# Kernel tuning notes

Hardware: AMD Instinct MI355X
Metric: run time of the kernel (lower is better)

The kernel has to match this reference:

```python
import jax, jax.numpy as jnp
import numpy as np

DIM = 192
NUM_HEADS = 6
WS = 8  # window size
N = WS * WS
HEAD_DIM = DIM // NUM_HEADS
SCALE = HEAD_DIM ** -0.5
B_ = 4096  # B * num_windows = 4 * (256/8)^2


def _relative_position_index(ws):
    # Static Swin relative-position index, computed with numpy at trace time.
    coords = np.stack(np.meshgrid(np.arange(ws), np.arange(ws), indexing='ij'))  # (2, ws, ws)
    flat = coords.reshape(2, -1)                       # (2, N)
    rel = flat[:, :, None] - flat[:, None, :]          # (2, N, N)
    rel = rel.transpose(1, 2, 0).astype(np.int64)      # (N, N, 2)
    rel[:, :, 0] += ws - 1
    rel[:, :, 1] += ws - 1
    rel[:, :, 0] *= 2 * ws - 1
    return np.clip(rel.sum(-1), -1000, 1000)           # (N, N)


_REL_IDX = _relative_position_index(WS)


def setup_inputs() -> dict:
    key = jax.random.key(0)
    ks = jax.random.split(key, 6)
    inv = 1.0 / np.sqrt(DIM)
    return {
        'x': jax.random.normal(ks[0], (B_, N, DIM), dtype=jnp.float32),
        'qkv_w': jax.random.normal(ks[1], (3 * DIM, DIM), dtype=jnp.float32) * inv,
        'qkv_b': jax.random.normal(ks[2], (3 * DIM,), dtype=jnp.float32) * 0.02,
        'proj_w': jax.random.normal(ks[3], (DIM, DIM), dtype=jnp.float32) * inv,
        'proj_b': jax.random.normal(ks[4], (DIM,), dtype=jnp.float32) * 0.02,
        'rel_bias_table': jax.random.normal(ks[5], ((2 * WS - 1) ** 2, NUM_HEADS), dtype=jnp.float32) * 0.02,
    }


def reference(x, qkv_w, qkv_b, proj_w, proj_b, rel_bias_table):
    B, n, C = x.shape  # (B_, 64, 192)
    # QKV projection (torch Linear: x @ W^T + b)
    qkv = x @ qkv_w.T + qkv_b                               # (B_, N, 3C)
    qkv = qkv.reshape(B, n, 3, NUM_HEADS, HEAD_DIM)
    qkv = jnp.transpose(qkv, (2, 0, 3, 1, 4))               # (3, B_, h, N, d)
    q, k, v = qkv[0], qkv[1], qkv[2]
    q = q * SCALE
    attn = jnp.einsum('bhnd,bhmd->bhnm', q, k)              # (B_, h, N, N)
    # relative position bias gather: (N*N,) -> (N, N, h) -> (h, N, N)
    bias = rel_bias_table[_REL_IDX.reshape(-1)].reshape(n, n, NUM_HEADS)
    attn = attn + jnp.transpose(bias, (2, 0, 1))[None]
    attn = jax.nn.softmax(attn, axis=-1)
    out = jnp.einsum('bhnm,bhmd->bhnd', attn, v)            # (B_, h, N, d)
    out = jnp.transpose(out, (0, 2, 1, 3)).reshape(B, n, C)
    out = out @ proj_w.T + proj_b
    return out
```

## Files before the change

kernel.cpp:

```cpp
#include <hip/hip_runtime.h>
#include <hip/hip_bf16.h>

#define NWIN 4096
#define NH 6
#define NTOK 64
#define CDIM 192
#define SCALE 0.17677669529663687f
#define LOG2E 1.4426950408889634f

typedef __attribute__((ext_vector_type(8))) short short8;
typedef __attribute__((ext_vector_type(4))) short short4v;
typedef __attribute__((ext_vector_type(4))) float f32x4;

#define MFMA32(A, B, C) __builtin_amdgcn_mfma_f32_16x16x32_bf16(A, B, C, 0, 0, 0)
#define MFMA16(A, B, C) __builtin_amdgcn_mfma_f32_16x16x16bf16_1k(A, B, C, 0, 0, 0)

__device__ __forceinline__ short bf(float x) {
  union { __hip_bfloat16 h; short s; } u;
  u.h = __float2bfloat16(x);
  return u.s;
}

__device__ __forceinline__ short8 cvt8v(f32x4 a, f32x4 b) {
  short8 r;
#pragma unroll
  for (int i = 0; i < 4; ++i) { r[i] = bf(a[i]); r[4 + i] = bf(b[i]); }
  return r;
}

__global__ void prep_weights(const float* __restrict__ qkv_w,
                             const float* __restrict__ proj_w,
                             const float* __restrict__ rel_tbl,
                             const float* __restrict__ qkv_b,
                             short* __restrict__ wbuf,
                             float* __restrict__ biasS,
                             float* __restrict__ qkvb2) {
  const int i = blockIdx.x * 256 + threadIdx.x;
  if (i < 110592) {
    float v = qkv_w[i];
    if (i < 36864) v *= SCALE * LOG2E;
    wbuf[i] = bf(v);
  } else if (i < 147456) {
    wbuf[i] = bf(proj_w[i - 110592]);
  } else if (i < 245760) {
    const int j = i - 147456;
    const int h = j >> 14;
    const int t = j & 16383;
    const int slot = t >> 10;
    const int ln = (t >> 2) & 63;
    const int e = t & 3;
    const int qh = slot >> 3, nl = (slot >> 2) & 1, mt = slot & 3;
    const int n = qh * 32 + nl * 16 + (ln & 15);
    const int m = mt * 16 + (ln >> 4) * 4 + e;
    const int idx = ((n >> 3) - (m >> 3) + 7) * 15 + ((n & 7) - (m & 7) + 7);
    biasS[j] = rel_tbl[idx * NH + h] * LOG2E;
  } else {
    const int j = i - 245760;
    if (j < 576) qkvb2[j] = qkv_b[j] * (j < CDIM ? SCALE * LOG2E : 1.0f);
  }
}

#define LDAF(dst, kc) do {                                              \
  _Pragma("unroll")                                                     \
  for (int mt_ = 0; mt_ < 4; ++mt_) {                                   \
    const int r_ = mt_ * 16 + cc;                                       \
    dst[mt_] = *(const short8*)&lds[r_ * CDIM + ((kc) ^ ((r_ & 7) << 3))]; \
  } } while (0)

__global__ __launch_bounds__(384, 3)
void swin_block_kernel(const float* __restrict__ x,
                       const short* __restrict__ wall,
                       const float* __restrict__ qkvb2,
                       const float* __restrict__ proj_b,
                       const float* __restrict__ biasS,
                       float* __restrict__ out) {
  __shared__ __align__(16) short lds[12288];

  const int b = blockIdx.x;
  const int tid = threadIdx.x;
  const int w = tid >> 6;
  const int lane = tid & 63;
  const int g = lane >> 4;
  const int cc = lane & 15;

  const float* xp = x + (size_t)b * (NTOK * CDIM);

  const int rq0 = (w * 32 + cc) * CDIM;
  const int rq1 = rq0 + 16 * CDIM;
  const short* wk_ = wall + CDIM * CDIM;
  const short* wv_ = wall + 2 * CDIM * CDIM;
  const short* wp_ = wall + 3 * CDIM * CDIM;

#pragma unroll
  for (int it = 0; it < 2; ++it) {
    const int flat = (tid + it * 384) * 16;
    const int r = flat / CDIM;
    const int c = flat % CDIM;
    const int X = (r & 7) << 3;
    f32x4 a0 = *(const f32x4*)(xp + flat);
    f32x4 a1 = *(const f32x4*)(xp + flat + 4);
    f32x4 a2 = *(const f32x4*)(xp + flat + 8);
    f32x4 a3 = *(const f32x4*)(xp + flat + 12);
    *(short8*)&lds[r * CDIM + (c ^ X)] = cvt8v(a0, a1);
    *(short8*)&lds[r * CDIM + ((c + 8) ^ X)] = cvt8v(a2, a3);
  }
  __syncthreads();

  short4v qf[4][2], kf[4][2];
  short4v vf[2][4];

  {
    f32x4 acc[2][4];
#pragma unroll
    for (int ft = 0; ft < 2; ++ft)
#pragma unroll
      for (int mt = 0; mt < 4; ++mt)
        acc[ft][mt] = (f32x4){0.f, 0.f, 0.f, 0.f};
#pragma unroll 1
    for (int ks = 0; ks < 6; ++ks) {
      const int c0 = ks * 32 + g * 8;
      short8 w0 = *(const short8*)&wall[rq0 + c0];
      short8 w1 = *(const short8*)&wall[rq1 + c0];
      short8 afr[4];
      LDAF(afr, c0);
#pragma unroll
      for (int mt = 0; mt < 4; ++mt) {
        acc[0][mt] = MFMA32(w0, afr[mt], acc[0][mt]);
        acc[1][mt] = MFMA32(w1, afr[mt], acc[1][mt]);
      }
    }
#pragma unroll
    for (int ft = 0; ft < 2; ++ft) {
      f32x4 qb = *(const f32x4*)&qkvb2[w * 32 + ft * 16 + g * 4];
#pragma unroll
      for (int nt = 0; nt < 4; ++nt)
#pragma unroll
        for (int j = 0; j < 4; ++j)
          qf[nt][ft][j] = bf(acc[ft][nt][j] + qb[j]);
    }
  }

  {
    f32x4 acc[2][4];
#pragma unroll
    for (int ft = 0; ft < 2; ++ft)
#pragma unroll
      for (int mt = 0; mt < 4; ++mt)
        acc[ft][mt] = (f32x4){0.f, 0.f, 0.f, 0.f};
#pragma unroll 1
    for (int ks = 0; ks < 6; ++ks) {
      const int c0 = ks * 32 + g * 8;
      short8 w0 = *(const short8*)&wk_[rq0 + c0];
      short8 w1 = *(const short8*)&wk_[rq1 + c0];
      short8 afr[4];
      LDAF(afr, c0);
#pragma unroll
      for (int mt = 0; mt < 4; ++mt) {
        acc[0][mt] = MFMA32(w0, afr[mt], acc[0][mt]);
        acc[1][mt] = MFMA32(w1, afr[mt], acc[1][mt]);
      }
    }
#pragma unroll
    for (int ft = 0; ft < 2; ++ft) {
      f32x4 kb = *(const f32x4*)&qkvb2[CDIM + w * 32 + ft * 16 + g * 4];
#pragma unroll
      for (int nt = 0; nt < 4; ++nt)
#pragma unroll
        for (int j = 0; j < 4; ++j)
          kf[nt][ft][j] = bf(acc[ft][nt][j] + kb[j]);
    }
  }

  {
    f32x4 acc[4][2];
#pragma unroll
    for (int mt = 0; mt < 4; ++mt)
#pragma unroll
      for (int dt = 0; dt < 2; ++dt)
        acc[mt][dt] = (f32x4){0.f, 0.f, 0.f, 0.f};
#pragma unroll 1
    for (int ks = 0; ks < 6; ++ks) {
      const int c0 = ks * 32 + g * 8;
      short8 w0 = *(const short8*)&wv_[rq0 + c0];
      short8 w1 = *(const short8*)&wv_[rq1 + c0];
      short8 afr[4];
      LDAF(afr, c0);
#pragma unroll
      for (int mt = 0; mt < 4; ++mt) {
        acc[mt][0] = MFMA32(afr[mt], w0, acc[mt][0]);
        acc[mt][1] = MFMA32(afr[mt], w1, acc[mt][1]);
      }
    }
    float vb0 = qkvb2[2 * CDIM + w * 32 + cc];
    float vb1 = qkvb2[2 * CDIM + w * 32 + 16 + cc];
#pragma unroll
    for (int kt = 0; kt < 4; ++kt)
#pragma unroll
      for (int j = 0; j < 4; ++j) {
        vf[0][kt][j] = bf(acc[kt][0][j] + vb0);
        vf[1][kt][j] = bf(acc[kt][1][j] + vb1);
      }
  }

  __syncthreads();

  const float* bs = biasS + w * 16384;
#pragma unroll
  for (int qh = 0; qh < 2; ++qh) {
    f32x4 sacc[4][2];
#pragma unroll
    for (int mt = 0; mt < 4; ++mt)
#pragma unroll
      for (int nl = 0; nl < 2; ++nl) {
        f32x4 z = *(const f32x4*)&bs[(((qh * 2 + nl) << 2) + mt) * 1024 + lane * 4];
        z = MFMA16(kf[mt][0], qf[qh * 2 + nl][0], z);
        sacc[mt][nl] = MFMA16(kf[mt][1], qf[qh * 2 + nl][1], z);
      }

    short4v pf[2][4];
#pragma unroll
    for (int nl = 0; nl < 2; ++nl) {
      float sum = 0.f;
#pragma unroll
      for (int mt = 0; mt < 4; ++mt)
#pragma unroll
        for (int e = 0; e < 4; ++e) {
          float p = exp2f(sacc[mt][nl][e]);
          sacc[mt][nl][e] = p;
          sum += p;
        }
      sum += __shfl_xor(sum, 16);
      sum += __shfl_xor(sum, 32);
      const float rinv = __builtin_amdgcn_rcpf(sum);
#pragma unroll
      for (int kt = 0; kt < 4; ++kt)
#pragma unroll
        for (int j = 0; j < 4; ++j)
          pf[nl][kt][j] = bf(sacc[kt][nl][j] * rinv);
    }

    f32x4 oacc[2][2];
#pragma unroll
    for (int nl = 0; nl < 2; ++nl)
#pragma unroll
      for (int dt = 0; dt < 2; ++dt) {
        f32x4 z = (f32x4){0.f, 0.f, 0.f, 0.f};
#pragma unroll
        for (int kt = 0; kt < 4; ++kt)
          z = MFMA16(pf[nl][kt], vf[dt][kt], z);
        oacc[nl][dt] = z;
      }

#pragma unroll
    for (int nl = 0; nl < 2; ++nl)
#pragma unroll
      for (int dt = 0; dt < 2; ++dt)
#pragma unroll
        for (int e = 0; e < 4; ++e) {
          const int r = qh * 32 + nl * 16 + g * 4 + e;
          const int c = w * 32 + dt * 16 + cc;
          lds[r * CDIM + (c ^ ((r & 7) << 3))] = bf(oacc[nl][dt][e]);
        }
  }
  __syncthreads();

  f32x4 pacc[4][2];
#pragma unroll
  for (int mt = 0; mt < 4; ++mt)
#pragma unroll
    for (int jt = 0; jt < 2; ++jt)
      pacc[mt][jt] = (f32x4){0.f, 0.f, 0.f, 0.f};

#pragma unroll 1
  for (int ks = 0; ks < 6; ++ks) {
    const int c0 = ks * 32 + g * 8;
    short8 p0 = *(const short8*)&wp_[rq0 + c0];
    short8 p1 = *(const short8*)&wp_[rq1 + c0];
    short8 afr[4];
    LDAF(afr, c0);
#pragma unroll
    for (int mt = 0; mt < 4; ++mt) {
      pacc[mt][0] = MFMA32(p0, afr[mt], pacc[mt][0]);
      pacc[mt][1] = MFMA32(p1, afr[mt], pacc[mt][1]);
    }
  }

  float* op = out + (size_t)b * (NTOK * CDIM);
  f32x4 pbv[2];
  pbv[0] = *(const f32x4*)&proj_b[w * 32 + g * 4];
  pbv[1] = *(const f32x4*)&proj_b[w * 32 + 16 + g * 4];
#pragma unroll
  for (int mt = 0; mt < 4; ++mt)
#pragma unroll
    for (int jt = 0; jt < 2; ++jt) {
      f32x4 v = pacc[mt][jt] + pbv[jt];
      *(f32x4*)&op[(mt * 16 + cc) * CDIM + w * 32 + jt * 16 + g * 4] = v;
    }
}

extern "C" void kernel_launch(void* const* d_in, const int* in_sizes, int n_in,
                              void* d_out, int out_size, void* d_ws, size_t ws_size,
                              hipStream_t stream) {
  const float* x       = (const float*)d_in[0];
  const float* qkv_w   = (const float*)d_in[1];
  const float* qkv_b   = (const float*)d_in[2];
  const float* proj_w  = (const float*)d_in[3];
  const float* proj_b  = (const float*)d_in[4];
  const float* rel_tbl = (const float*)d_in[5];
  float* out = (float*)d_out;

  short* wbuf  = (short*)d_ws;
  float* biasS = (float*)(wbuf + 147456);
  float* qkvb2 = biasS + 98304;

  prep_weights<<<963, 256, 0, stream>>>(qkv_w, proj_w, rel_tbl, qkv_b,
                                        wbuf, biasS, qkvb2);
  swin_block_kernel<<<NWIN, 384, 0, stream>>>(x, wbuf, qkvb2, proj_b, biasS, out);
}
```

Measured before the change: 274.7 us.

## Halve block to three waves, each wave processing two heads with software overlap

The fused Swin window-attention block now uses 192 threads (3 waves) instead of 384, with each wave computing QKV and attention for two heads. The second head's QKV projection is issued before the LDS barrier, so it can overlap with the first head's attention results held in registers. The output projection gives each wave 64 output columns. The aim is to raise blocks per CU and reuse the LDS A-fragments across more MFMAs. The cost is higher register pressure and less parallelism within each block.

```diff
diff --git a/kernel.cpp b/kernel.cpp
--- a/kernel.cpp
+++ b/kernel.cpp
@@ -67,7 +67,176 @@
     dst[mt_] = *(const short8*)&lds[r_ * CDIM + ((kc) ^ ((r_ & 7) << 3))]; \
   } } while (0)
 
-__global__ __launch_bounds__(384, 3)
+__device__ __forceinline__ void stage1_head(
+    const short* lds, const short* wall, const float* qkvb2,
+    int h, int cc, int g,
+    short4v qf[4][2], short4v kf[4][2], short4v vf[2][4]) {
+  const short* wk_ = wall + CDIM * CDIM;
+  const short* wv_ = wall + 2 * CDIM * CDIM;
+  const int r0 = (h * 32 + cc) * CDIM;
+  const int r1 = r0 + 16 * CDIM;
+
+  {
+    f32x4 acc[2][4];
+#pragma unroll
+    for (int ft = 0; ft < 2; ++ft)
+#pragma unroll
+      for (int mt = 0; mt < 4; ++mt)
+        acc[ft][mt] = (f32x4){0.f, 0.f, 0.f, 0.f};
+#pragma unroll 1
+    for (int ks = 0; ks < 6; ++ks) {
+      const int c0 = ks * 32 + g * 8;
+      short8 w0 = *(const short8*)&wall[r0 + c0];
+      short8 w1 = *(const short8*)&wall[r1 + c0];
+      short8 afr[4];
+      LDAF(afr, c0);
+#pragma unroll
+      for (int mt = 0; mt < 4; ++mt) {
+        acc[0][mt] = MFMA32(w0, afr[mt], acc[0][mt]);
+        acc[1][mt] = MFMA32(w1, afr[mt], acc[1][mt]);
+      }
+    }
+#pragma unroll
+    for (int ft = 0; ft < 2; ++ft) {
+      f32x4 qb = *(const f32x4*)&qkvb2[h * 32 + ft * 16 + g * 4];
+#pragma unroll
+      for (int nt = 0; nt < 4; ++nt)
+#pragma unroll
+        for (int j = 0; j < 4; ++j)
+          qf[nt][ft][j] = bf(acc[ft][nt][j] + qb[j]);
+    }
+  }
+  {
+    f32x4 acc[2][4];
+#pragma unroll
+    for (int ft = 0; ft < 2; ++ft)
+#pragma unroll
+      for (int mt = 0; mt < 4; ++mt)
+        acc[ft][mt] = (f32x4){0.f, 0.f, 0.f, 0.f};
+#pragma unroll 1
+    for (int ks = 0; ks < 6; ++ks) {
+      const int c0 = ks * 32 + g * 8;
+      short8 w0 = *(const short8*)&wk_[r0 + c0];
+      short8 w1 = *(const short8*)&wk_[r1 + c0];
+      short8 afr[4];
+      LDAF(afr, c0);
+#pragma unroll
+      for (int mt = 0; mt < 4; ++mt) {
+        acc[0][mt] = MFMA32(w0, afr[mt], acc[0][mt]);
+        acc[1][mt] = MFMA32(w1, afr[mt], acc[1][mt]);
+      }
+    }
+#pragma unroll
+    for (int ft = 0; ft < 2; ++ft) {
+      f32x4 kb = *(const f32x4*)&qkvb2[CDIM + h * 32 + ft * 16 + g * 4];
+#pragma unroll
+      for (int nt = 0; nt < 4; ++nt)
+#pragma unroll
+        for (int j = 0; j < 4; ++j)
+          kf[nt][ft][j] = bf(acc[ft][nt][j] + kb[j]);
+    }
+  }
+  {
+    f32x4 acc[4][2];
+#pragma unroll
+    for (int mt = 0; mt < 4; ++mt)
+#pragma unroll
+      for (int dt = 0; dt < 2; ++dt)
+        acc[mt][dt] = (f32x4){0.f, 0.f, 0.f, 0.f};
+#pragma unroll 1
+    for (int ks = 0; ks < 6; ++ks) {
+      const int c0 = ks * 32 + g * 8;
+      short8 w0 = *(const short8*)&wv_[r0 + c0];
+      short8 w1 = *(const short8*)&wv_[r1 + c0];
+      short8 afr[4];
+      LDAF(afr, c0);
+#pragma unroll
+      for (int mt = 0; mt < 4; ++mt) {
+        acc[mt][0] = MFMA32(afr[mt], w0, acc[mt][0]);
+        acc[mt][1] = MFMA32(afr[mt], w1, acc[mt][1]);
+      }
+    }
+    float vb0 = qkvb2[2 * CDIM + h * 32 + cc];
+    float vb1 = qkvb2[2 * CDIM + h * 32 + 16 + cc];
+#pragma unroll
+    for (int kt = 0; kt < 4; ++kt)
+#pragma unroll
+      for (int j = 0; j < 4; ++j) {
+        vf[0][kt][j] = bf(acc[kt][0][j] + vb0);
+        vf[1][kt][j] = bf(acc[kt][1][j] + vb1);
+      }
+  }
+}
+
+__device__ __forceinline__ void attn_head(
+    const float* biasS, int h, int lane,
+    const short4v qf[4][2], const short4v kf[4][2], const short4v vf[2][4],
+    short4v o[2][2][2]) {
+  const float* bs = biasS + h * 16384;
+#pragma unroll
+  for (int qh = 0; qh < 2; ++qh) {
+    f32x4 sacc[4][2];
+#pragma unroll
+    for (int mt = 0; mt < 4; ++mt)
+#pragma unroll
+      for (int nl = 0; nl < 2; ++nl) {
+        f32x4 z = *(const f32x4*)&bs[(((qh * 2 + nl) << 2) + mt) * 1024 + lane * 4];
+        z = MFMA16(kf[mt][0], qf[qh * 2 + nl][0], z);
+        sacc[mt][nl] = MFMA16(kf[mt][1], qf[qh * 2 + nl][1], z);
+      }
+    short4v pf[2][4];
+#pragma unroll
+    for (int nl = 0; nl < 2; ++nl) {
+      float sum = 0.f;
+#pragma unroll
+      for (int mt = 0; mt < 4; ++mt)
+#pragma unroll
+        for (int e = 0; e < 4; ++e) {
+          float p = exp2f(sacc[mt][nl][e]);
+          sacc[mt][nl][e] = p;
+          sum += p;
+        }
+      sum += __shfl_xor(sum, 16);
+      sum += __shfl_xor(sum, 32);
+      const float rinv = __builtin_amdgcn_rcpf(sum);
+#pragma unroll
+      for (int kt = 0; kt < 4; ++kt)
+#pragma unroll
+        for (int j = 0; j < 4; ++j)
+          pf[nl][kt][j] = bf(sacc[kt][nl][j] * rinv);
+    }
+#pragma unroll
+    for (int nl = 0; nl < 2; ++nl)
+#pragma unroll
+      for (int dt = 0; dt < 2; ++dt) {
+        f32x4 z = (f32x4){0.f, 0.f, 0.f, 0.f};
+#pragma unroll
+        for (int kt = 0; kt < 4; ++kt)
+          z = MFMA16(pf[nl][kt], vf[dt][kt], z);
+#pragma unroll
+        for (int e = 0; e < 4; ++e)
+          o[qh][nl][dt][e] = bf(z[e]);
+      }
+  }
+}
+
+__device__ __forceinline__ void write_ao(short* lds, int h, int g, int cc,
+                                         const short4v o[2][2][2]) {
+#pragma unroll
+  for (int qh = 0; qh < 2; ++qh)
+#pragma unroll
+    for (int nl = 0; nl < 2; ++nl)
+#pragma unroll
+      for (int dt = 0; dt < 2; ++dt)
+#pragma unroll
+        for (int e = 0; e < 4; ++e) {
+          const int r = qh * 32 + nl * 16 + g * 4 + e;
+          const int c = h * 32 + dt * 16 + cc;
+          lds[r * CDIM + (c ^ ((r & 7) << 3))] = o[qh][nl][dt][e];
+        }
+}
+
+__global__ __launch_bounds__(192, 4)
 void swin_block_kernel(const float* __restrict__ x,
                        const short* __restrict__ wall,
                        const float* __restrict__ qkvb2,
@@ -78,22 +247,17 @@
 
   const int b = blockIdx.x;
   const int tid = threadIdx.x;
-  const int w = tid >> 6;
+  const int wv = tid >> 6;
   const int lane = tid & 63;
   const int g = lane >> 4;
   const int cc = lane & 15;
+  const int h0 = wv * 2;
 
   const float* xp = x + (size_t)b * (NTOK * CDIM);
 
-  const int rq0 = (w * 32 + cc) * CDIM;
-  const int rq1 = rq0 + 16 * CDIM;
-  const short* wk_ = wall + CDIM * CDIM;
-  const short* wv_ = wall + 2 * CDIM * CDIM;
-  const short* wp_ = wall + 3 * CDIM * CDIM;
-
-#pragma unroll
-  for (int it = 0; it < 2; ++it) {
-    const int flat = (tid + it * 384) * 16;
+#pragma unroll
+  for (int it = 0; it < 4; ++it) {
+    const int flat = (tid + it * 192) * 16;
     const int r = flat / CDIM;
     const int c = flat % CDIM;
     const int X = (r & 7) << 3;
@@ -106,195 +270,64 @@
   }
   __syncthreads();
 
-  short4v qf[4][2], kf[4][2];
-  short4v vf[2][4];
-
-  {
-    f32x4 acc[2][4];
-#pragma unroll
-    for (int ft = 0; ft < 2; ++ft)
-#pragma unroll
-      for (int mt = 0; mt < 4; ++mt)
-        acc[ft][mt] = (f32x4){0.f, 0.f, 0.f, 0.f};
-#pragma unroll 1
-    for (int ks = 0; ks < 6; ++ks) {
-      const int c0 = ks * 32 + g * 8;
-      short8 w0 = *(const short8*)&wall[rq0 + c0];
-      short8 w1 = *(const short8*)&wall[rq1 + c0];
-      short8 afr[4];
-      LDAF(afr, c0);
-#pragma unroll
-      for (int mt = 0; mt < 4; ++mt) {
-        acc[0][mt] = MFMA32(w0, afr[mt], acc[0][mt]);
-        acc[1][mt] = MFMA32(w1, afr[mt], acc[1][mt]);
-      }
-    }
-#pragma unroll
-    for (int ft = 0; ft < 2; ++ft) {
-      f32x4 qb = *(const f32x4*)&qkvb2[w * 32 + ft * 16 + g * 4];
-#pragma unroll
-      for (int nt = 0; nt < 4; ++nt)
-#pragma unroll
-        for (int j = 0; j < 4; ++j)
-          qf[nt][ft][j] = bf(acc[ft][nt][j] + qb[j]);
-    }
-  }
-
-  {
-    f32x4 acc[2][4];
-#pragma unroll
-    for (int ft = 0; ft < 2; ++ft)
-#pragma unroll
-      for (int mt = 0; mt < 4; ++mt)
-        acc[ft][mt] = (f32x4){0.f, 0.f, 0.f, 0.f};
-#pragma unroll 1
-    for (int ks = 0; ks < 6; ++ks) {
-      const int c0 = ks * 32 + g * 8;
-      short8 w0 = *(const short8*)&wk_[rq0 + c0];
-      short8 w1 = *(const short8*)&wk_[rq1 + c0];
-      short8 afr[4];
-      LDAF(afr, c0);
-#pragma unroll
-      for (int mt = 0; mt < 4; ++mt) {
-        acc[0][mt] = MFMA32(w0, afr[mt], acc[0][mt]);
-        acc[1][mt] = MFMA32(w1, afr[mt], acc[1][mt]);
-      }
-    }
-#pragma unroll
-    for (int ft = 0; ft < 2; ++ft) {
-      f32x4 kb = *(const f32x4*)&qkvb2[CDIM + w * 32 + ft * 16 + g * 4];
-#pragma unroll
-      for (int nt = 0; nt < 4; ++nt)
-#pragma unroll
-        for (int j = 0; j < 4; ++j)
-          kf[nt][ft][j] = bf(acc[ft][nt][j] + kb[j]);
-    }
-  }
-
-  {
-    f32x4 acc[4][2];
-#pragma unroll
-    for (int mt = 0; mt < 4; ++mt)
-#pragma unroll
-      for (int dt = 0; dt < 2; ++dt)
-        acc[mt][dt] = (f32x4){0.f, 0.f, 0.f, 0.f};
-#pragma unroll 1
-    for (int ks = 0; ks < 6; ++ks) {
-      const int c0 = ks * 32 + g * 8;
-      short8 w0 = *(const short8*)&wv_[rq0 + c0];
-      short8 w1 = *(const short8*)&wv_[rq1 + c0];
-      short8 afr[4];
-      LDAF(afr, c0);
-#pragma unroll
-      for (int mt = 0; mt < 4; ++mt) {
-        acc[mt][0] = MFMA32(afr[mt], w0, acc[mt][0]);
-        acc[mt][1] = MFMA32(afr[mt], w1, acc[mt][1]);
-      }
-    }
-    float vb0 = qkvb2[2 * CDIM + w * 32 + cc];
-    float vb1 = qkvb2[2 * CDIM + w * 32 + 16 + cc];
-#pragma unroll
-    for (int kt = 0; kt < 4; ++kt)
-#pragma unroll
-      for (int j = 0; j < 4; ++j) {
-        vf[0][kt][j] = bf(acc[kt][0][j] + vb0);
-        vf[1][kt][j] = bf(acc[kt][1][j] + vb1);
-      }
-  }
+  short4v oA[2][2][2];
+  {
+    short4v qf[4][2], kf[4][2], vf[2][4];
+    stage1_head(lds, wall, qkvb2, h0, cc, g, qf, kf, vf);
+    attn_head(biasS, h0, lane, qf, kf, vf, oA);
+  }
+
+  short4v qfB[4][2], kfB[4][2], vfB[2][4];
+  stage1_head(lds, wall, qkvb2, h0 + 1, cc, g, qfB, kfB, vfB);
 
   __syncthreads();
 
-  const float* bs = biasS + w * 16384;
-#pragma unroll
-  for (int qh = 0; qh < 2; ++qh) {
-    f32x4 sacc[4][2];
-#pragma unroll
-    for (int mt = 0; mt < 4; ++mt)
-#pragma unroll
-      for (int nl = 0; nl < 2; ++nl) {
-        f32x4 z = *(const f32x4*)&bs[(((qh * 2 + nl) << 2) + mt) * 1024 + lane * 4];
-        z = MFMA16(kf[mt][0], qf[qh * 2 + nl][0], z);
-        sacc[mt][nl] = MFMA16(kf[mt][1], qf[qh * 2 + nl][1], z);
-      }
-
-    short4v pf[2][4];
-#pragma unroll
-    for (int nl = 0; nl < 2; ++nl) {
-      float sum = 0.f;
-#pragma unroll
-      for (int mt = 0; mt < 4; ++mt)
-#pragma unroll
-        for (int e = 0; e < 4; ++e) {
-          float p = exp2f(sacc[mt][nl][e]);
-          sacc[mt][nl][e] = p;
-          sum += p;
-        }
-      sum += __shfl_xor(sum, 16);
-      sum += __shfl_xor(sum, 32);
-      const float rinv = __builtin_amdgcn_rcpf(sum);
-#pragma unroll
-      for (int kt = 0; kt < 4; ++kt)
-#pragma unroll
-        for (int j = 0; j < 4; ++j)
-          pf[nl][kt][j] = bf(sacc[kt][nl][j] * rinv);
-    }
-
-    f32x4 oacc[2][2];
-#pragma unroll
-    for (int nl = 0; nl < 2; ++nl)
-#pragma unroll
-      for (int dt = 0; dt < 2; ++dt) {
-        f32x4 z = (f32x4){0.f, 0.f, 0.f, 0.f};
-#pragma unroll
-        for (int kt = 0; kt < 4; ++kt)
-          z = MFMA16(pf[nl][kt], vf[dt][kt], z);
-        oacc[nl][dt] = z;
-      }
-
-#pragma unroll
-    for (int nl = 0; nl < 2; ++nl)
-#pragma unroll
-      for (int dt = 0; dt < 2; ++dt)
-#pragma unroll
-        for (int e = 0; e < 4; ++e) {
-          const int r = qh * 32 + nl * 16 + g * 4 + e;
-          const int c = w * 32 + dt * 16 + cc;
-          lds[r * CDIM + (c ^ ((r & 7) << 3))] = bf(oacc[nl][dt][e]);
-        }
+  write_ao(lds, h0, g, cc, oA);
+  {
+    short4v oB[2][2][2];
+    attn_head(biasS, h0 + 1, lane, qfB, kfB, vfB, oB);
+    write_ao(lds, h0 + 1, g, cc, oB);
   }
   __syncthreads();
 
-  f32x4 pacc[4][2];
+  const short* wp_ = wall + 3 * CDIM * CDIM;
+  const int rp0 = (wv * 64 + cc) * CDIM;
+  f32x4 pacc[4][4];
 #pragma unroll
   for (int mt = 0; mt < 4; ++mt)
 #pragma unroll
-    for (int jt = 0; jt < 2; ++jt)
+    for (int jt = 0; jt < 4; ++jt)
       pacc[mt][jt] = (f32x4){0.f, 0.f, 0.f, 0.f};
 
 #pragma unroll 1
   for (int ks = 0; ks < 6; ++ks) {
     const int c0 = ks * 32 + g * 8;
-    short8 p0 = *(const short8*)&wp_[rq0 + c0];
-    short8 p1 = *(const short8*)&wp_[rq1 + c0];
+    short8 p0 = *(const short8*)&wp_[rp0 + c0];
+    short8 p1 = *(const short8*)&wp_[rp0 + 16 * CDIM + c0];
+    short8 p2 = *(const short8*)&wp_[rp0 + 32 * CDIM + c0];
+    short8 p3 = *(const short8*)&wp_[rp0 + 48 * CDIM + c0];
     short8 afr[4];
     LDAF(afr, c0);
 #pragma unroll
     for (int mt = 0; mt < 4; ++mt) {
       pacc[mt][0] = MFMA32(p0, afr[mt], pacc[mt][0]);
       pacc[mt][1] = MFMA32(p1, afr[mt], pacc[mt][1]);
+      pacc[mt][2] = MFMA32(p2, afr[mt], pacc[mt][2]);
+      pacc[mt][3] = MFMA32(p3, afr[mt], pacc[mt][3]);
     }
   }
 
   float* op = out + (size_t)b * (NTOK * CDIM);
-  f32x4 pbv[2];
-  pbv[0] = *(const f32x4*)&proj_b[w * 32 + g * 4];
-  pbv[1] = *(const f32x4*)&proj_b[w * 32 + 16 + g * 4];
+  f32x4 pbv[4];
+#pragma unroll
+  for (int jt = 0; jt < 4; ++jt)
+    pbv[jt] = *(const f32x4*)&proj_b[wv * 64 + jt * 16 + g * 4];
 #pragma unroll
   for (int mt = 0; mt < 4; ++mt)
 #pragma unroll
-    for (int jt = 0; jt < 2; ++jt) {
+    for (int jt = 0; jt < 4; ++jt) {
       f32x4 v = pacc[mt][jt] + pbv[jt];
-      *(f32x4*)&op[(mt * 16 + cc) * CDIM + w * 32 + jt * 16 + g * 4] = v;
+      *(f32x4*)&op[(mt * 16 + cc) * CDIM + wv * 64 + jt * 16 + g * 4] = v;
     }
 }
 
@@ -315,5 +348,5 @@
 
   prep_weights<<<963, 256, 0, stream>>>(qkv_w, proj_w, rel_tbl, qkv_b,
                                         wbuf, biasS, qkvb2);
-  swin_block_kernel<<<NWIN, 384, 0, stream>>>(x, wbuf, qkvb2, proj_b, biasS, out);
-}
+  swin_block_kernel<<<NWIN, 192, 0, stream>>>(x, wbuf, qkvb2, proj_b, biasS, out);
+}
```

New measurement: 295.6 us. 7.6% more time.
